# Kernel tuning notes

Hardware: AMD Instinct MI355X
Metric: run time of the kernel (lower is better)

## Reference

```python
import jax, jax.numpy as jnp
import numpy as np

B = 4096   # per-view batch size
D = 256    # projection dim
TEMPERATURE = 0.1
EPS = 1e-12  # F.normalize eps


def setup_inputs() -> dict:
    key = jax.random.key(0)
    kq, kk = jax.random.split(key)
    features_q = jax.random.normal(kq, (B, D), dtype=jnp.float32)
    features_k = jax.random.normal(kk, (B, D), dtype=jnp.float32)
    return {"features_q": features_q, "features_k": features_k}


def _neg_index_matrix(n):
    # Static (numpy) construction of the per-row negative column indices:
    # row i keeps all columns except i (diagonal) and its positive partner.
    rows = np.arange(n)
    partner = (rows + n // 2) % n
    cols = np.broadcast_to(np.arange(n), (n, n))
    keep = (cols != rows[:, None]) & (cols != partner[:, None])
    return cols[keep].reshape(n, n - 2), partner


def reference(features_q, features_k):
    f = jnp.concatenate([features_q, features_k], axis=0)      # [2B, D]
    norm = jnp.maximum(jnp.linalg.norm(f, axis=1, keepdims=True), EPS)
    f = f / norm
    sim = f @ f.T                                              # [2B, 2B]

    n = 2 * B
    neg_idx_np, partner_np = _neg_index_matrix(n)
    rows = jnp.arange(n)
    partner = jnp.asarray(partner_np)
    pos = sim[rows, partner]                                   # [2B]
    neg = jnp.take_along_axis(sim, jnp.asarray(neg_idx_np), axis=1)  # [2B, 2B-2]

    logits = jnp.concatenate([pos[:, None], neg], axis=1) / TEMPERATURE
    # CrossEntropyLoss with label 0 for every row, mean reduction:
    loss = jnp.mean(jax.nn.logsumexp(logits, axis=1) - logits[:, 0])
    return loss
```

## Files before the change

kernel.cpp:

```cpp
#include <hip/hip_runtime.h>
#include <hip/hip_bf16.h>
#include <math.h>

#define N_TOTAL 8192
#define D_DIM   256
#define INV_T   10.0f
#define BM 128
#define BN 128
#define BK 32
#define K_ITERS (D_DIM / BK)
#define NT 64

typedef __bf16 bf16_8 __attribute__((ext_vector_type(8)));
typedef float  f32x4  __attribute__((ext_vector_type(4)));

typedef const __attribute__((address_space(1))) unsigned int* gptr_t;
typedef __attribute__((address_space(3))) unsigned int*       lptr_t;

__device__ __forceinline__ void gload16(const void* g, void* l) {
    __builtin_amdgcn_global_load_lds((gptr_t)g, (lptr_t)l, 16, 0, 0);
}

__device__ __forceinline__ unsigned short f2bf(float f) {
    unsigned int u = __float_as_uint(f);
    return (unsigned short)((u + 0x7FFFu + ((u >> 16) & 1u)) >> 16);
}

__global__ __launch_bounds__(256) void normalize_kernel(
    const float* __restrict__ q, const float* __restrict__ k,
    unsigned short* __restrict__ F, float* __restrict__ out)
{
    if (blockIdx.x == 0 && threadIdx.x == 0) out[0] = 0.f;
    int row  = blockIdx.x * 4 + (threadIdx.x >> 6);
    int lane = threadIdx.x & 63;
    const float* src = (row < 4096) ? (q + (size_t)row * D_DIM)
                                    : (k + (size_t)(row - 4096) * D_DIM);
    float4 v = ((const float4*)src)[lane];
    float ss = v.x*v.x + v.y*v.y + v.z*v.z + v.w*v.w;
    #pragma unroll
    for (int off = 32; off > 0; off >>= 1) ss += __shfl_xor(ss, off, 64);
    float inv = 1.0f / fmaxf(sqrtf(ss), 1e-12f);
    ushort4 o;
    o.x = f2bf(v.x * inv); o.y = f2bf(v.y * inv);
    o.z = f2bf(v.z * inv); o.w = f2bf(v.w * inv);
    ((ushort4*)(F + (size_t)row * D_DIM))[lane] = o;
}

__device__ __forceinline__ int tri_off(int x) { return x * NT - (x * (x - 1)) / 2; }

__global__ __launch_bounds__(256) void simloss_gemm(
    const __hip_bfloat16* __restrict__ F,
    float* __restrict__ partial, float* __restrict__ pos)
{
    __shared__ __hip_bfloat16 As[2][BM * BK];
    __shared__ __hip_bfloat16 Bs[2][BN * BK];
    __shared__ float s_row[BM];
    __shared__ float s_col[BN];

    int b  = blockIdx.x;
    int bx = (int)(64.5f - sqrtf(64.5f * 64.5f - 2.0f * (float)b));
    if (bx < 0) bx = 0; if (bx > NT - 1) bx = NT - 1;
    while (bx > 0 && tri_off(bx) > b) --bx;
    while (bx < NT - 1 && tri_off(bx + 1) <= b) ++bx;
    const int by = bx + (b - tri_off(bx));
    const bool is_diag = (bx == by);

    const int i0 = bx * BM;
    const int j0 = by * BN;
    const int tid  = threadIdx.x;
    const int wave = tid >> 6;
    const int lane = tid & 63;
    const int wm = (wave & 1) * 64;
    const int wn = (wave >> 1) * 64;
    const int g  = lane >> 4;
    const int cj = lane & 15;

    if (tid < BM) { s_row[tid] = 0.f; s_col[tid] = 0.f; }

    f32x4 acc[4][4];
    #pragma unroll
    for (int a = 0; a < 4; ++a)
        #pragma unroll
        for (int c = 0; c < 4; ++c)
            acc[a][c] = (f32x4){0.f, 0.f, 0.f, 0.f};

    #define STAGE(buf, kk)                                                        \
        _Pragma("unroll")                                                         \
        for (int p = 0; p < 2; ++p) {                                             \
            gload16(F + (size_t)(i0 + p * 64 + lane) * D_DIM + (kk) + wave * 8,   \
                    &As[buf][(wave * 128 + p * 64) * 8]);                         \
            gload16(F + (size_t)(j0 + p * 64 + lane) * D_DIM + (kk) + wave * 8,   \
                    &Bs[buf][(wave * 128 + p * 64) * 8]);                         \
        }

    STAGE(0, 0);
    int cur = 0;
    for (int kk = 0; kk < K_ITERS; ++kk) {
        if (kk + 1 < K_ITERS) {
            STAGE(cur ^ 1, (kk + 1) * BK);
            asm volatile("s_waitcnt vmcnt(4)" ::: "memory");
        } else {
            asm volatile("s_waitcnt vmcnt(0)" ::: "memory");
        }
        __builtin_amdgcn_s_barrier();

        bf16_8 a[4], bfr[4];
        #pragma unroll
        for (int t = 0; t < 4; ++t) {
            a[t]   = *(const bf16_8*)(&As[cur][(g * 128 + wm + t * 16 + cj) * 8]);
            bfr[t] = *(const bf16_8*)(&Bs[cur][(g * 128 + wn + t * 16 + cj) * 8]);
        }
        #pragma unroll
        for (int ti = 0; ti < 4; ++ti)
            #pragma unroll
            for (int tj = 0; tj < 4; ++tj)
                acc[ti][tj] = __builtin_amdgcn_mfma_f32_16x16x32_bf16(
                    a[ti], bfr[tj], acc[ti][tj], 0, 0, 0);

        __builtin_amdgcn_s_barrier();
        cur ^= 1;
    }
    #undef STAGE

    float colsum[4] = {0.f, 0.f, 0.f, 0.f};
    #pragma unroll
    for (int ti = 0; ti < 4; ++ti) {
        #pragma unroll
        for (int r = 0; r < 4; ++r) {
            const int i = i0 + wm + ti * 16 + g * 4 + r;
            const int partner = (i + 4096) & (N_TOTAL - 1);
            float esum = 0.f;
            #pragma unroll
            for (int tj = 0; tj < 4; ++tj) {
                const int j = j0 + wn + tj * 16 + cj;
                const float v = acc[ti][tj][r];
                float e = __expf(v * INV_T);
                if (is_diag && j == i) e = 0.f;
                if (!is_diag && j == partner) {
                    pos[i] = v; pos[j] = v;
                }
                esum += e;
                colsum[tj] += e;
            }
            #pragma unroll
            for (int off = 1; off < 16; off <<= 1)
                esum += __shfl_xor(esum, off, 64);
            if (cj == 0) atomicAdd(&s_row[wm + ti * 16 + g * 4 + r], esum);
        }
    }
    if (!is_diag) {
        #pragma unroll
        for (int tj = 0; tj < 4; ++tj) {
            float cs = colsum[tj];
            cs += __shfl_xor(cs, 16, 64);
            cs += __shfl_xor(cs, 32, 64);
            if (g == 0) atomicAdd(&s_col[wn + tj * 16 + cj], cs);
        }
    }
    __syncthreads();

    if (tid < BM) {
        partial[(size_t)by * N_TOTAL + i0 + tid] = s_row[tid];
    } else if (!is_diag) {
        partial[(size_t)bx * N_TOTAL + j0 + (tid - BM)] = s_col[tid - BM];
    }
}

__global__ __launch_bounds__(256) void finalize_kernel(
    const float* __restrict__ partial, const float* __restrict__ pos,
    float* __restrict__ out)
{
    const int row = blockIdx.x * 256 + threadIdx.x;
    float s = 0.f;
    #pragma unroll 8
    for (int t = 0; t < NT; ++t)
        s += partial[(size_t)t * N_TOTAL + row];
    float v = logf(s) - pos[row] * INV_T;
    #pragma unroll
    for (int off = 32; off > 0; off >>= 1) v += __shfl_xor(v, off, 64);
    __shared__ float wsum[4];
    if ((threadIdx.x & 63) == 0) wsum[threadIdx.x >> 6] = v;
    __syncthreads();
    if (threadIdx.x == 0)
        atomicAdd(out, (wsum[0] + wsum[1] + wsum[2] + wsum[3]) * (1.0f / N_TOTAL));
}

extern "C" void kernel_launch(void* const* d_in, const int* in_sizes, int n_in,
                              void* d_out, int out_size, void* d_ws, size_t ws_size,
                              hipStream_t stream) {
    const float* q = (const float*)d_in[0];
    const float* k = (const float*)d_in[1];
    float* out = (float*)d_out;

    char* ws = (char*)d_ws;
    const size_t f_bytes = (size_t)N_TOTAL * D_DIM * sizeof(unsigned short);
    const size_t p_bytes = (size_t)NT * N_TOTAL * sizeof(float);
    unsigned short* F = (unsigned short*)ws;
    float* partial = (float*)(ws + f_bytes);
    float* pos     = (float*)(ws + f_bytes + p_bytes);

    normalize_kernel<<<N_TOTAL / 4, 256, 0, stream>>>(q, k, F, out);
    simloss_gemm<<<NT * (NT + 1) / 2, 256, 0, stream>>>((const __hip_bfloat16*)F, partial, pos);
    finalize_kernel<<<32, 256, 0, stream>>>(partial, pos, out);
}
```

Baseline: 115.3 us.

## Fuse normalize, GEMM-loss and finalize into one cooperative persistent kernel

```diff
diff --git a/kernel.cpp b/kernel.cpp
--- a/kernel.cpp
+++ b/kernel.cpp
@@ -1,4 +1,5 @@
 #include <hip/hip_runtime.h>
+#include <hip/hip_cooperative_groups.h>
 #include <hip/hip_bf16.h>
 #include <math.h>
 
@@ -10,6 +11,10 @@
 #define BK 32
 #define K_ITERS (D_DIM / BK)
 #define NT 64
+#define N_TILES (NT * (NT + 1) / 2)
+#define GRID 512
+
+namespace cg = cooperative_groups;
 
 typedef __bf16 bf16_8 __attribute__((ext_vector_type(8)));
 typedef float  f32x4  __attribute__((ext_vector_type(4)));
@@ -24,6 +29,165 @@
 __device__ __forceinline__ unsigned short f2bf(float f) {
     unsigned int u = __float_as_uint(f);
     return (unsigned short)((u + 0x7FFFu + ((u >> 16) & 1u)) >> 16);
+}
+
+__device__ __forceinline__ int tri_off(int x) { return x * NT - (x * (x - 1)) / 2; }
+
+__global__ __launch_bounds__(256) void fused_all(
+    const float* __restrict__ qin, const float* __restrict__ kin,
+    unsigned short* __restrict__ Fu, float* __restrict__ partial,
+    float* __restrict__ pos, float* __restrict__ out)
+{
+    const __hip_bfloat16* F = (const __hip_bfloat16*)Fu;
+    __shared__ __hip_bfloat16 As[2][BM * BK];
+    __shared__ __hip_bfloat16 Bs[2][BN * BK];
+    __shared__ float s_row[BM];
+    __shared__ float s_col[BN];
+
+    const int tid  = threadIdx.x;
+    const int wave = tid >> 6;
+    const int lane = tid & 63;
+
+    if (blockIdx.x == 0 && tid == 0) out[0] = 0.f;
+    for (int vb = blockIdx.x; vb < N_TOTAL / 4; vb += GRID) {
+        const int row = vb * 4 + wave;
+        const float* src = (row < 4096) ? (qin + (size_t)row * D_DIM)
+                                        : (kin + (size_t)(row - 4096) * D_DIM);
+        float4 v = ((const float4*)src)[lane];
+        float ss = v.x*v.x + v.y*v.y + v.z*v.z + v.w*v.w;
+        #pragma unroll
+        for (int off = 32; off > 0; off >>= 1) ss += __shfl_xor(ss, off, 64);
+        float inv = 1.0f / fmaxf(sqrtf(ss), 1e-12f);
+        ushort4 o;
+        o.x = f2bf(v.x * inv); o.y = f2bf(v.y * inv);
+        o.z = f2bf(v.z * inv); o.w = f2bf(v.w * inv);
+        ((ushort4*)(Fu + (size_t)row * D_DIM))[lane] = o;
+    }
+    cg::this_grid().sync();
+
+    const int wm = (wave & 1) * 64;
+    const int wn = (wave >> 1) * 64;
+    const int g  = lane >> 4;
+    const int cj = lane & 15;
+
+    for (int b = blockIdx.x; b < N_TILES; b += GRID) {
+        int bx = (int)(64.5f - sqrtf(64.5f * 64.5f - 2.0f * (float)b));
+        if (bx < 0) bx = 0; if (bx > NT - 1) bx = NT - 1;
+        while (bx > 0 && tri_off(bx) > b) --bx;
+        while (bx < NT - 1 && tri_off(bx + 1) <= b) ++bx;
+        const int by = bx + (b - tri_off(bx));
+        const bool is_diag = (bx == by);
+        const int i0 = bx * BM;
+        const int j0 = by * BN;
+
+        if (tid < BM) { s_row[tid] = 0.f; s_col[tid] = 0.f; }
+
+        f32x4 acc[4][4];
+        #pragma unroll
+        for (int a = 0; a < 4; ++a)
+            #pragma unroll
+            for (int c = 0; c < 4; ++c)
+                acc[a][c] = (f32x4){0.f, 0.f, 0.f, 0.f};
+
+        #define STAGE(buf, kk)                                                        \
+            _Pragma("unroll")                                                         \
+            for (int p = 0; p < 2; ++p) {                                             \
+                gload16(F + (size_t)(i0 + p * 64 + lane) * D_DIM + (kk) + wave * 8,   \
+                        &As[buf][(wave * 128 + p * 64) * 8]);                         \
+                gload16(F + (size_t)(j0 + p * 64 + lane) * D_DIM + (kk) + wave * 8,   \
+                        &Bs[buf][(wave * 128 + p * 64) * 8]);                         \
+            }
+
+        STAGE(0, 0);
+        int cur = 0;
+        for (int kk = 0; kk < K_ITERS; ++kk) {
+            if (kk + 1 < K_ITERS) {
+                STAGE(cur ^ 1, (kk + 1) * BK);
+                asm volatile("s_waitcnt vmcnt(4)" ::: "memory");
+            } else {
+                asm volatile("s_waitcnt vmcnt(0)" ::: "memory");
+            }
+            __builtin_amdgcn_s_barrier();
+
+            bf16_8 a[4], bfr[4];
+            #pragma unroll
+            for (int t = 0; t < 4; ++t) {
+                a[t]   = *(const bf16_8*)(&As[cur][(g * 128 + wm + t * 16 + cj) * 8]);
+                bfr[t] = *(const bf16_8*)(&Bs[cur][(g * 128 + wn + t * 16 + cj) * 8]);
+            }
+            #pragma unroll
+            for (int ti = 0; ti < 4; ++ti)
+                #pragma unroll
+                for (int tj = 0; tj < 4; ++tj)
+                    acc[ti][tj] = __builtin_amdgcn_mfma_f32_16x16x32_bf16(
+                        a[ti], bfr[tj], acc[ti][tj], 0, 0, 0);
+
+            __builtin_amdgcn_s_barrier();
+            cur ^= 1;
+        }
+        #undef STAGE
+
+        float colsum[4] = {0.f, 0.f, 0.f, 0.f};
+        #pragma unroll
+        for (int ti = 0; ti < 4; ++ti) {
+            #pragma unroll
+            for (int r = 0; r < 4; ++r) {
+                const int i = i0 + wm + ti * 16 + g * 4 + r;
+                const int partner = (i + 4096) & (N_TOTAL - 1);
+                float esum = 0.f;
+                #pragma unroll
+                for (int tj = 0; tj < 4; ++tj) {
+                    const int j = j0 + wn + tj * 16 + cj;
+                    const float v = acc[ti][tj][r];
+                    float e = __expf(v * INV_T);
+                    if (is_diag && j == i) e = 0.f;
+                    if (!is_diag && j == partner) {
+                        pos[i] = v; pos[j] = v;
+                    }
+                    esum += e;
+                    colsum[tj] += e;
+                }
+                #pragma unroll
+                for (int off = 1; off < 16; off <<= 1)
+                    esum += __shfl_xor(esum, off, 64);
+                if (cj == 0) atomicAdd(&s_row[wm + ti * 16 + g * 4 + r], esum);
+            }
+        }
+        if (!is_diag) {
+            #pragma unroll
+            for (int tj = 0; tj < 4; ++tj) {
+                float cs = colsum[tj];
+                cs += __shfl_xor(cs, 16, 64);
+                cs += __shfl_xor(cs, 32, 64);
+                if (g == 0) atomicAdd(&s_col[wn + tj * 16 + cj], cs);
+            }
+        }
+        __syncthreads();
+
+        if (tid < BM) {
+            partial[(size_t)by * N_TOTAL + i0 + tid] = s_row[tid];
+        } else if (!is_diag) {
+            partial[(size_t)bx * N_TOTAL + j0 + (tid - BM)] = s_col[tid - BM];
+        }
+        __syncthreads();
+    }
+    cg::this_grid().sync();
+
+    if (blockIdx.x < N_TOTAL / 256) {
+        const int row = blockIdx.x * 256 + tid;
+        float s = 0.f;
+        #pragma unroll 8
+        for (int t = 0; t < NT; ++t)
+            s += partial[(size_t)t * N_TOTAL + row];
+        float v = logf(s) - pos[row] * INV_T;
+        #pragma unroll
+        for (int off = 32; off > 0; off >>= 1) v += __shfl_xor(v, off, 64);
+        __shared__ float wsum[4];
+        if (lane == 0) wsum[wave] = v;
+        __syncthreads();
+        if (tid == 0)
+            atomicAdd(out, (wsum[0] + wsum[1] + wsum[2] + wsum[3]) * (1.0f / N_TOTAL));
+    }
 }
 
 __global__ __launch_bounds__(256) void normalize_kernel(
@@ -46,8 +210,6 @@
     ((ushort4*)(F + (size_t)row * D_DIM))[lane] = o;
 }
 
-__device__ __forceinline__ int tri_off(int x) { return x * NT - (x * (x - 1)) / 2; }
-
 __global__ __launch_bounds__(256) void simloss_gemm(
     const __hip_bfloat16* __restrict__ F,
     float* __restrict__ partial, float* __restrict__ pos)
@@ -136,9 +298,7 @@
                 const float v = acc[ti][tj][r];
                 float e = __expf(v * INV_T);
                 if (is_diag && j == i) e = 0.f;
-                if (!is_diag && j == partner) {
-                    pos[i] = v; pos[j] = v;
-                }
+                if (!is_diag && j == partner) { pos[i] = v; pos[j] = v; }
                 esum += e;
                 colsum[tj] += e;
             }
@@ -199,7 +359,13 @@
     float* partial = (float*)(ws + f_bytes);
     float* pos     = (float*)(ws + f_bytes + p_bytes);
 
-    normalize_kernel<<<N_TOTAL / 4, 256, 0, stream>>>(q, k, F, out);
-    simloss_gemm<<<NT * (NT + 1) / 2, 256, 0, stream>>>((const __hip_bfloat16*)F, partial, pos);
-    finalize_kernel<<<32, 256, 0, stream>>>(partial, pos, out);
-}
+    void* args[] = { (void*)&q, (void*)&k, (void*)&F,
+                     (void*)&partial, (void*)&pos, (void*)&out };
+    hipError_t err = hipLaunchCooperativeKernel(
+        (const void*)fused_all, dim3(GRID), dim3(256), args, 0, stream);
+    if (err != hipSuccess) {
+        normalize_kernel<<<N_TOTAL / 4, 256, 0, stream>>>(q, k, F, out);
+        simloss_gemm<<<N_TILES, 256, 0, stream>>>((const __hip_bfloat16*)F, partial, pos);
+        finalize_kernel<<<32, 256, 0, stream>>>(partial, pos, out);
+    }
+}
```

Measured after the change: 225.2 us. 95.4% more time.
